# Optimization experiments

Hardware: AMD Instinct MI355X
Metric: run time of the kernel (lower is better)

## Reference

```python
import jax, jax.numpy as jnp
import numpy as np

B, S, H = 128, 512, 256
STEP = 1


def setup_inputs() -> dict:
    key = jax.random.key(0)
    ks = jax.random.split(key, 16)
    stdv = 1.0 / np.sqrt(H)
    u = lambda k, shape: jax.random.uniform(k, shape, jnp.float32, -stdv, stdv)
    return {
        "A": jax.random.uniform(ks[0], (B, S, 2 * S), jnp.float32),
        "hidden": jax.random.normal(ks[1], (B, S, H), jnp.float32),
        "mask": jnp.ones((B, S), jnp.int32),
        # linear_edge_in / linear_edge_out (Linear(H, H, bias=True))
        "W_in": u(ks[2], (H, H)),  "b_in": u(ks[3], (H,)),
        "W_out": u(ks[4], (H, H)), "b_out": u(ks[5], (H,)),
        # adjacency biases
        "b_iah": u(ks[6], (H,)), "b_oah": u(ks[7], (H,)),
        # GRU-style gate weights: w_ih [3H, 2H], w_hh [3H, H]
        "w_ih": u(ks[8], (3 * H, 2 * H)), "b_ih": u(ks[9], (3 * H,)),
        "w_hh": u(ks[10], (3 * H, H)),    "b_hh": u(ks[11], (3 * H,)),
    }


def _gnn_cell(A, hidden, W_in, b_in, W_out, b_out, b_iah, b_oah,
              w_ih, b_ih, w_hh, b_hh):
    s = hidden.shape[1]
    # edge-transformed features (torch F.linear: x @ W.T + b)
    h_in = jnp.einsum('bsh,gh->bsg', hidden, W_in) + b_in
    h_out = jnp.einsum('bsh,gh->bsg', hidden, W_out) + b_out
    # adjacency message passing: [B,S,S] @ [B,S,H]
    input_in = jnp.einsum('bij,bjh->bih', A[:, :, :s], h_in) + b_iah
    input_out = jnp.einsum('bij,bjh->bih', A[:, :, s:2 * s], h_out) + b_oah
    inputs = jnp.concatenate([input_in, input_out], axis=2)  # [B,S,2H]
    gi = jnp.einsum('bsi,gi->bsg', inputs, w_ih) + b_ih      # [B,S,3H]
    gh = jnp.einsum('bsh,gh->bsg', hidden, w_hh) + b_hh      # [B,S,3H]
    i_r, i_i, i_n = jnp.split(gi, 3, axis=2)
    h_r, h_i, h_n = jnp.split(gh, 3, axis=2)
    resetgate = jax.nn.sigmoid(i_r + h_r)
    inputgate = jax.nn.sigmoid(i_i + h_i)
    newgate = jnp.tanh(i_n + resetgate * h_n)
    return hidden + inputgate * (newgate - hidden)


def reference(A, hidden, mask, W_in, b_in, W_out, b_out, b_iah, b_oah,
              w_ih, b_ih, w_hh, b_hh):
    # GNN.forward with issrgnn=True: run GNNCell `step` times (mask unused)
    for _ in range(STEP):
        hidden = _gnn_cell(A, hidden, W_in, b_in, W_out, b_out,
                           b_iah, b_oah, w_ih, b_ih, w_hh, b_hh)
    return hidden
```

## Files before the change

kernel.cpp:

```cpp
#include <hip/hip_runtime.h>

#define B_ 128
#define S_ 512
#define H_ 256
#define M_ (B_*S_)

typedef __attribute__((ext_vector_type(4))) float f32x4;
typedef __attribute__((ext_vector_type(8))) short s16x8;
typedef __attribute__((ext_vector_type(4))) unsigned short u16x4;
typedef unsigned short ushort_t;

typedef __attribute__((address_space(1))) void as1_void;
typedef __attribute__((address_space(3))) void as3_void;

__device__ __forceinline__ unsigned short f2h(float f) {
  _Float16 h = (_Float16)f;
  return __builtin_bit_cast(unsigned short, h);
}

__device__ __forceinline__ f32x4 mfma16(s16x8 a, s16x8 b, f32x4 c) {
  asm("v_mfma_f32_16x16x32_f16 %0, %1, %2, %0" : "+v"(c) : "v"(a), "v"(b));
  return c;
}

__device__ __forceinline__ void cp16(const void* g, void* l) {
  __builtin_amdgcn_global_load_lds((as1_void*)g, (as3_void*)l, 16, 0, 0);
}

__device__ __forceinline__ void waitvm(int n) {
  switch (n) {
    case 0:  asm volatile("s_waitcnt vmcnt(0)"  ::: "memory"); break;
    case 4:  asm volatile("s_waitcnt vmcnt(4)"  ::: "memory"); break;
    case 5:  asm volatile("s_waitcnt vmcnt(5)"  ::: "memory"); break;
    case 6:  asm volatile("s_waitcnt vmcnt(6)"  ::: "memory"); break;
    case 8:  asm volatile("s_waitcnt vmcnt(8)"  ::: "memory"); break;
    case 12: asm volatile("s_waitcnt vmcnt(12)" ::: "memory"); break;
  }
}

__device__ __forceinline__ int stage_kc(int lane) {
  return (lane & 3) ^ ((lane >> 3) & 3);
}
__device__ __forceinline__ int frag_off(int s, int lane) {
  int ln = lane & 15, kg = lane >> 4;
  return s * 512 + (ln * 4 + (kg ^ ((ln >> 1) & 3))) * 8;
}

__global__ void k_cvt_f16(const float* __restrict__ in, ushort_t* __restrict__ out, int n8) {
  int i = blockIdx.x * blockDim.x + threadIdx.x;
  if (i >= n8) return;
  const float* p = in + (size_t)i * 8;
  f32x4 a = *(const f32x4*)p;
  f32x4 b = *(const f32x4*)(p + 4);
  s16x8 o;
  o[0]=(short)f2h(a[0]); o[1]=(short)f2h(a[1]); o[2]=(short)f2h(a[2]); o[3]=(short)f2h(a[3]);
  o[4]=(short)f2h(b[0]); o[5]=(short)f2h(b[1]); o[6]=(short)f2h(b[2]); o[7]=(short)f2h(b[3]);
  *(s16x8*)(out + (size_t)i * 8) = o;
}

__global__ __launch_bounds__(256, 2)
void k_gemm1(const ushort_t* __restrict__ hid, const ushort_t* __restrict__ wcat,
             const float* __restrict__ b_in, const float* __restrict__ b_out,
             ushort_t* __restrict__ hcatT) {
  __shared__ __attribute__((aligned(16))) ushort_t lA[3][8*512];
  __shared__ __attribute__((aligned(16))) ushort_t lB[3][16*512];
  const int flat = blockIdx.y * 8 + blockIdx.x;
  const int orig = (flat & 7) * 128 + (flat >> 3);
  const int bx = orig & 7, bb = orig >> 3;
  const int j0 = (bx >> 1) * 128;
  const int n0 = (bx & 1) * 256;
  const int tid = threadIdx.x;
  const int w = tid >> 6, lane = tid & 63;
  const int ln = lane & 15, kg = lane >> 4;
  const int wm = w >> 1, wn = w & 1;
  const int srow = lane >> 2, skc = stage_kc(lane);

  f32x4 acc[4][8];
  #pragma unroll
  for (int i = 0; i < 4; ++i)
    #pragma unroll
    for (int j = 0; j < 8; ++j) acc[i][j] = (f32x4){0.f,0.f,0.f,0.f};

  const size_t arow0 = (size_t)bb * 512 + j0;

  auto stage = [&](int t, int bsel) {
    int k0 = t * 32;
    #pragma unroll
    for (int it = 0; it < 2; ++it) {
      int s = it*4 + w;
      cp16(hid + (arow0 + s*16 + srow)*256 + k0 + skc*8, &lA[bsel][s*512]);
    }
    #pragma unroll
    for (int it = 0; it < 4; ++it) {
      int s = it*4 + w;
      cp16(wcat + (size_t)(n0 + s*16 + srow)*256 + k0 + skc*8, &lB[bsel][s*512]);
    }
  };
  auto compute = [&](int cur) {
    s16x8 af[4];
    #pragma unroll
    for (int mf = 0; mf < 4; ++mf)
      af[mf] = *(const s16x8*)&lA[cur][frag_off(wm*4 + mf, lane)];
    __builtin_amdgcn_s_setprio(1);
    #pragma unroll
    for (int nf = 0; nf < 8; ++nf) {
      s16x8 bf = *(const s16x8*)&lB[cur][frag_off(wn*8 + nf, lane)];
      #pragma unroll
      for (int mf = 0; mf < 4; ++mf) acc[mf][nf] = mfma16(af[mf], bf, acc[mf][nf]);
    }
    __builtin_amdgcn_s_setprio(0);
  };

  stage(0, 0); stage(1, 1);
  for (int t = 0; t < 6; ++t) {
    waitvm(6);
    __builtin_amdgcn_s_barrier();
    stage(t + 2, (t + 2) % 3);
    compute(t % 3);
  }
  waitvm(6); __builtin_amdgcn_s_barrier(); compute(6 % 3);
  waitvm(0); __builtin_amdgcn_s_barrier(); compute(7 % 3);

  #pragma unroll
  for (int nf = 0; nf < 8; ++nf) {
    int gn = n0 + wn*128 + nf*16 + ln;
    float bias = (gn < 256) ? b_in[gn] : b_out[gn - 256];
    #pragma unroll
    for (int mf = 0; mf < 4; ++mf) {
      int j = j0 + wm*64 + mf*16 + kg*4;
      u16x4 v;
      #pragma unroll
      for (int r = 0; r < 4; ++r) v[r] = f2h(acc[mf][nf][r] + bias);
      *(u16x4*)&hcatT[((size_t)(bb*512 + gn))*512 + j] = v;
    }
  }
}

__global__ __launch_bounds__(256, 2)
void k_gemm2(const float* __restrict__ A, const ushort_t* __restrict__ hcatT,
             const float* __restrict__ b_iah, const float* __restrict__ b_oah,
             ushort_t* __restrict__ inp) {
  __shared__ __attribute__((aligned(16))) ushort_t lA[2][8*512];
  __shared__ __attribute__((aligned(16))) ushort_t lB[3][16*512];
  const int flat = blockIdx.y * 8 + blockIdx.x;
  const int orig = (flat & 7) * 128 + (flat >> 3);
  const int bx = orig & 7, bb = orig >> 3;
  const int i0 = (bx >> 1) * 128;
  const int half = bx & 1;
  const int n0 = half * 256;
  const int tid = threadIdx.x;
  const int w = tid >> 6, lane = tid & 63;
  const int ln = lane & 15, kg = lane >> 4;
  const int wm = w >> 1, wn = w & 1;
  const int srow = lane >> 2, skc = stage_kc(lane);

  f32x4 acc[4][8];
  #pragma unroll
  for (int i = 0; i < 4; ++i)
    #pragma unroll
    for (int j = 0; j < 8; ++j) acc[i][j] = (f32x4){0.f,0.f,0.f,0.f};

  const float* Abase = A + ((size_t)bb*512 + i0)*1024 + half*512;
  f32x4 ra[2][4];

  auto loadA = [&](int t, f32x4 (&r)[4]) {
    int k0 = t * 32;
    #pragma unroll
    for (int it = 0; it < 2; ++it) {
      int s = it*4 + w;
      const float* p = Abase + (size_t)(s*16 + srow)*1024 + k0 + skc*8;
      r[it*2]   = *(const f32x4*)p;
      r[it*2+1] = *(const f32x4*)(p + 4);
    }
  };
  auto stageB = [&](int t, int bsel) {
    int k0 = t * 32;
    #pragma unroll
    for (int it = 0; it < 4; ++it) {
      int s = it*4 + w;
      cp16(hcatT + ((size_t)(bb*512 + n0 + s*16 + srow))*512 + k0 + skc*8, &lB[bsel][s*512]);
    }
  };
  auto writeA = [&](const f32x4 (&r)[4], int bsel) {
    #pragma unroll
    for (int it = 0; it < 2; ++it) {
      int s = it*4 + w;
      s16x8 o;
      o[0]=(short)f2h(r[it*2][0]); o[1]=(short)f2h(r[it*2][1]);
      o[2]=(short)f2h(r[it*2][2]); o[3]=(short)f2h(r[it*2][3]);
      o[4]=(short)f2h(r[it*2+1][0]); o[5]=(short)f2h(r[it*2+1][1]);
      o[6]=(short)f2h(r[it*2+1][2]); o[7]=(short)f2h(r[it*2+1][3]);
      *(s16x8*)&lA[bsel][s*512 + lane*8] = o;
    }
  };
  auto compute = [&](int acur, int bcur) {
    s16x8 af[4];
    #pragma unroll
    for (int mf = 0; mf < 4; ++mf)
      af[mf] = *(const s16x8*)&lA[acur][frag_off(wm*4 + mf, lane)];
    __builtin_amdgcn_s_setprio(1);
    #pragma unroll
    for (int nf = 0; nf < 8; ++nf) {
      s16x8 bf = *(const s16x8*)&lB[bcur][frag_off(wn*8 + nf, lane)];
      #pragma unroll
      for (int mf = 0; mf < 4; ++mf) acc[mf][nf] = mfma16(af[mf], bf, acc[mf][nf]);
    }
    __builtin_amdgcn_s_setprio(0);
  };

  loadA(0, ra[0]); stageB(0, 0);
  loadA(1, ra[1]); stageB(1, 1);
  waitvm(12);
  writeA(ra[0], 0);
  asm volatile("s_waitcnt lgkmcnt(0)" ::: "memory");

  #pragma unroll
  for (int t = 0; t < 16; ++t) {
    waitvm(t < 15 ? 8 : 0);
    __builtin_amdgcn_s_barrier();
    if (t + 2 < 16) { loadA(t + 2, ra[t & 1]); stageB(t + 2, (t + 2) % 3); }
    compute(t & 1, t % 3);
    if (t + 1 < 16) {
      waitvm(t + 2 < 16 ? 12 : 4);
      writeA(ra[(t + 1) & 1], (t + 1) & 1);
      asm volatile("s_waitcnt lgkmcnt(0)" ::: "memory");
    }
  }

  #pragma unroll
  for (int nf = 0; nf < 8; ++nf) {
    int gn = n0 + wn*128 + nf*16 + ln;
    float bias = half ? b_oah[gn - 256] : b_iah[gn];
    #pragma unroll
    for (int mf = 0; mf < 4; ++mf) {
      #pragma unroll
      for (int r = 0; r < 4; ++r) {
        int i = i0 + wm*64 + mf*16 + kg*4 + r;
        inp[((size_t)(bb*512 + i))*512 + gn] = f2h(acc[mf][nf][r] + bias);
      }
    }
  }
}

__global__ __launch_bounds__(256, 2)
void k_gemm3(const ushort_t* __restrict__ inp, const ushort_t* __restrict__ hidh,
             const ushort_t* __restrict__ wih, const ushort_t* __restrict__ whh,
             const float* __restrict__ b_ih, const float* __restrict__ b_hh,
             const float* __restrict__ hidden, float* __restrict__ out) {
  __shared__ __attribute__((aligned(16))) ushort_t lIn[3][8*512];
  __shared__ __attribute__((aligned(16))) ushort_t lW[3][12*512];
  const int flat = blockIdx.y * 4 + blockIdx.x;
  const int orig = (flat & 7) * 256 + (flat >> 3);
  const int h0 = (orig & 3) * 64;
  const int m0 = (orig >> 2) * 128;
  const int tid = threadIdx.x;
  const int w = tid >> 6, lane = tid & 63;
  const int ln = lane & 15, kg = lane >> 4;
  const int wm2 = w >> 1, wh = w & 1;
  const int srow = lane >> 2, skc = stage_kc(lane);

  f32x4 aR[4][2], aI[4][2], aIN[4][2], aHN[4][2];
  #pragma unroll
  for (int m = 0; m < 4; ++m)
    #pragma unroll
    for (int n = 0; n < 2; ++n) {
      aR[m][n] = (f32x4){0.f,0.f,0.f,0.f}; aI[m][n] = (f32x4){0.f,0.f,0.f,0.f};
      aIN[m][n] = (f32x4){0.f,0.f,0.f,0.f}; aHN[m][n] = (f32x4){0.f,0.f,0.f,0.f};
    }

  auto stage = [&](int gs, int bsel) {
    if (gs < 16) {
      int k0 = gs * 32;
      #pragma unroll
      for (int it = 0; it < 2; ++it) {
        int s = it*4 + w;
        cp16(inp + (size_t)(m0 + s*16 + srow)*512 + k0 + skc*8, &lIn[bsel][s*512]);
      }
      #pragma unroll
      for (int it = 0; it < 3; ++it) {
        int s = it*4 + w;
        int row = s*16 + srow, g = row >> 6, r = row & 63;
        cp16(wih + (size_t)(g*256 + h0 + r)*512 + k0 + skc*8, &lW[bsel][s*512]);
      }
    } else {
      int k0 = (gs - 16) * 32;
      #pragma unroll
      for (int it = 0; it < 2; ++it) {
        int s = it*4 + w;
        cp16(hidh + (size_t)(m0 + s*16 + srow)*256 + k0 + skc*8, &lIn[bsel][s*512]);
      }
      #pragma unroll
      for (int it = 0; it < 3; ++it) {
        int s = it*4 + w;
        int row = s*16 + srow, g = row >> 6, r = row & 63;
        cp16(whh + (size_t)(g*256 + h0 + r)*256 + k0 + skc*8, &lW[bsel][s*512]);
      }
    }
  };

  auto compute = [&](int cur, f32x4 (&aN)[4][2]) {
    s16x8 af[4];
    #pragma unroll
    for (int mf = 0; mf < 4; ++mf)
      af[mf] = *(const s16x8*)&lIn[cur][frag_off(wm2*4 + mf, lane)];
    __builtin_amdgcn_s_setprio(1);
    #pragma unroll
    for (int g = 0; g < 3; ++g) {
      #pragma unroll
      for (int nf = 0; nf < 2; ++nf) {
        s16x8 bf = *(const s16x8*)&lW[cur][frag_off(g*4 + wh*2 + nf, lane)];
        #pragma unroll
        for (int mf = 0; mf < 4; ++mf) {
          f32x4& a = (g == 0 ? aR[mf][nf] : g == 1 ? aI[mf][nf] : aN[mf][nf]);
          a = mfma16(af[mf], bf, a);
        }
      }
    }
    __builtin_amdgcn_s_setprio(0);
  };

  stage(0, 0);
  stage(1, 1);
  for (int t = 0; t < 16; ++t) {
    waitvm(5);
    __builtin_amdgcn_s_barrier();
    stage(t + 2, (t + 2) % 3);
    compute(t % 3, aIN);
  }
  for (int t = 16; t < 22; ++t) {
    waitvm(5);
    __builtin_amdgcn_s_barrier();
    stage(t + 2, (t + 2) % 3);
    compute(t % 3, aHN);
  }
  waitvm(5); __builtin_amdgcn_s_barrier(); compute(22 % 3, aHN);
  waitvm(0); __builtin_amdgcn_s_barrier(); compute(23 % 3, aHN);

  #pragma unroll
  for (int nf = 0; nf < 2; ++nf) {
    int h = h0 + wh*32 + nf*16 + ln;
    float br  = b_ih[h]       + b_hh[h];
    float bi  = b_ih[256 + h] + b_hh[256 + h];
    float bni = b_ih[512 + h];
    float bnh = b_hh[512 + h];
    #pragma unroll
    for (int mf = 0; mf < 4; ++mf) {
      #pragma unroll
      for (int r = 0; r < 4; ++r) {
        int m = m0 + wm2*64 + mf*16 + kg*4 + r;
        float rg = 1.0f / (1.0f + __expf(-(aR[mf][nf][r] + br)));
        float ig = 1.0f / (1.0f + __expf(-(aI[mf][nf][r] + bi)));
        float narg = aIN[mf][nf][r] + bni + rg * (aHN[mf][nf][r] + bnh);
        float e2 = __expf(2.0f * narg);
        float ng = 1.0f - 2.0f / (e2 + 1.0f);
        float hv = hidden[(size_t)m*256 + h];
        out[(size_t)m*256 + h] = hv + ig * (ng - hv);
      }
    }
  }
}

extern "C" void kernel_launch(void* const* d_in, const int* in_sizes, int n_in,
                              void* d_out, int out_size, void* d_ws, size_t ws_size,
                              hipStream_t stream) {
  const float* A      = (const float*)d_in[0];
  const float* hidden = (const float*)d_in[1];
  const float* W_in   = (const float*)d_in[3];
  const float* b_in   = (const float*)d_in[4];
  const float* W_out  = (const float*)d_in[5];
  const float* b_out  = (const float*)d_in[6];
  const float* b_iah  = (const float*)d_in[7];
  const float* b_oah  = (const float*)d_in[8];
  const float* w_ih   = (const float*)d_in[9];
  const float* b_ih   = (const float*)d_in[10];
  const float* w_hh   = (const float*)d_in[11];
  const float* b_hh   = (const float*)d_in[12];
  float* out = (float*)d_out;

  char* ws = (char*)d_ws;
  ushort_t* hidh  = (ushort_t*)(ws);
  ushort_t* wcat  = (ushort_t*)(ws + 33554432);
  ushort_t* wihh  = (ushort_t*)(ws + 33816576);
  ushort_t* whhh  = (ushort_t*)(ws + 34603008);
  ushort_t* hcatT = (ushort_t*)(ws + 34996224);
  ushort_t* inp   = (ushort_t*)(ws + 102105088);

  k_cvt_f16<<<8192, 256, 0, stream>>>(hidden, hidh, M_*H_/8);
  k_cvt_f16<<<32,   256, 0, stream>>>(W_in,  wcat,           H_*H_/8);
  k_cvt_f16<<<32,   256, 0, stream>>>(W_out, wcat + H_*H_,   H_*H_/8);
  k_cvt_f16<<<192,  256, 0, stream>>>(w_ih,  wihh, 768*512/8);
  k_cvt_f16<<<96,   256, 0, stream>>>(w_hh,  whhh, 768*256/8);

  k_gemm1<<<dim3(8, 128), 256, 0, stream>>>(hidh, wcat, b_in, b_out, hcatT);
  k_gemm2<<<dim3(8, 128), 256, 0, stream>>>(A, hcatT, b_iah, b_oah, inp);
  k_gemm3<<<dim3(4, 512), 256, 0, stream>>>(inp, hidh, wihh, whhh, b_ih, b_hh, hidden, out);
}
```

Before: 283.4 us.

## Halve gemm3 N-tile to 32 hidden columns and merge conversion kernels into one launch

Measured after the change: 286.5 us. About the same (+1.1%).

```diff
diff --git a/kernel.cpp b/kernel.cpp
--- a/kernel.cpp
+++ b/kernel.cpp
@@ -30,6 +30,7 @@
 __device__ __forceinline__ void waitvm(int n) {
   switch (n) {
     case 0:  asm volatile("s_waitcnt vmcnt(0)"  ::: "memory"); break;
+    case 3:  asm volatile("s_waitcnt vmcnt(3)"  ::: "memory"); break;
     case 4:  asm volatile("s_waitcnt vmcnt(4)"  ::: "memory"); break;
     case 5:  asm volatile("s_waitcnt vmcnt(5)"  ::: "memory"); break;
     case 6:  asm volatile("s_waitcnt vmcnt(6)"  ::: "memory"); break;
@@ -46,16 +47,26 @@
   return s * 512 + (ln * 4 + (kg ^ ((ln >> 1) & 3))) * 8;
 }
 
-__global__ void k_cvt_f16(const float* __restrict__ in, ushort_t* __restrict__ out, int n8) {
-  int i = blockIdx.x * blockDim.x + threadIdx.x;
-  if (i >= n8) return;
-  const float* p = in + (size_t)i * 8;
+__global__ void k_cvt_all(const float* __restrict__ hidden, ushort_t* __restrict__ hidh,
+                          const float* __restrict__ W_in,  const float* __restrict__ W_out,
+                          ushort_t* __restrict__ wcat,
+                          const float* __restrict__ w_ih, ushort_t* __restrict__ wihh,
+                          const float* __restrict__ w_hh, ushort_t* __restrict__ whhh) {
+  int blk = blockIdx.x;
+  const float* src; ushort_t* dst; int base;
+  if (blk < 8192)      { src = hidden; dst = hidh;           base = blk; }
+  else if (blk < 8224) { src = W_in;   dst = wcat;           base = blk - 8192; }
+  else if (blk < 8256) { src = W_out;  dst = wcat + 65536;   base = blk - 8224; }
+  else if (blk < 8448) { src = w_ih;   dst = wihh;           base = blk - 8256; }
+  else                 { src = w_hh;   dst = whhh;           base = blk - 8448; }
+  int i = base * 256 + threadIdx.x;
+  const float* p = src + (size_t)i * 8;
   f32x4 a = *(const f32x4*)p;
   f32x4 b = *(const f32x4*)(p + 4);
   s16x8 o;
   o[0]=(short)f2h(a[0]); o[1]=(short)f2h(a[1]); o[2]=(short)f2h(a[2]); o[3]=(short)f2h(a[3]);
   o[4]=(short)f2h(b[0]); o[5]=(short)f2h(b[1]); o[6]=(short)f2h(b[2]); o[7]=(short)f2h(b[3]);
-  *(s16x8*)(out + (size_t)i * 8) = o;
+  *(s16x8*)(dst + (size_t)i * 8) = o;
 }
 
 __global__ __launch_bounds__(256, 2)
@@ -242,31 +253,29 @@
   }
 }
 
-__global__ __launch_bounds__(256, 2)
+__global__ __launch_bounds__(256, 3)
 void k_gemm3(const ushort_t* __restrict__ inp, const ushort_t* __restrict__ hidh,
              const ushort_t* __restrict__ wih, const ushort_t* __restrict__ whh,
              const float* __restrict__ b_ih, const float* __restrict__ b_hh,
              const float* __restrict__ hidden, float* __restrict__ out) {
   __shared__ __attribute__((aligned(16))) ushort_t lIn[3][8*512];
-  __shared__ __attribute__((aligned(16))) ushort_t lW[3][12*512];
-  const int flat = blockIdx.y * 4 + blockIdx.x;
-  const int orig = (flat & 7) * 256 + (flat >> 3);
-  const int h0 = (orig & 3) * 64;
-  const int m0 = (orig >> 2) * 128;
+  __shared__ __attribute__((aligned(16))) ushort_t lW[3][6*512];
+  const int flat = blockIdx.y * 8 + blockIdx.x;
+  const int orig = (flat & 7) * 512 + (flat >> 3);
+  const int h0 = (orig & 7) * 32;
+  const int m0 = (orig >> 3) * 128;
   const int tid = threadIdx.x;
   const int w = tid >> 6, lane = tid & 63;
   const int ln = lane & 15, kg = lane >> 4;
   const int wm2 = w >> 1, wh = w & 1;
   const int srow = lane >> 2, skc = stage_kc(lane);
 
-  f32x4 aR[4][2], aI[4][2], aIN[4][2], aHN[4][2];
-  #pragma unroll
-  for (int m = 0; m < 4; ++m)
-    #pragma unroll
-    for (int n = 0; n < 2; ++n) {
-      aR[m][n] = (f32x4){0.f,0.f,0.f,0.f}; aI[m][n] = (f32x4){0.f,0.f,0.f,0.f};
-      aIN[m][n] = (f32x4){0.f,0.f,0.f,0.f}; aHN[m][n] = (f32x4){0.f,0.f,0.f,0.f};
-    }
+  f32x4 aR[4], aI[4], aIN[4], aHN[4];
+  #pragma unroll
+  for (int m = 0; m < 4; ++m) {
+    aR[m] = (f32x4){0.f,0.f,0.f,0.f}; aI[m] = (f32x4){0.f,0.f,0.f,0.f};
+    aIN[m] = (f32x4){0.f,0.f,0.f,0.f}; aHN[m] = (f32x4){0.f,0.f,0.f,0.f};
+  }
 
   auto stage = [&](int gs, int bsel) {
     if (gs < 16) {
@@ -277,10 +286,12 @@
         cp16(inp + (size_t)(m0 + s*16 + srow)*512 + k0 + skc*8, &lIn[bsel][s*512]);
       }
       #pragma unroll
-      for (int it = 0; it < 3; ++it) {
+      for (int it = 0; it < 2; ++it) {
         int s = it*4 + w;
-        int row = s*16 + srow, g = row >> 6, r = row & 63;
-        cp16(wih + (size_t)(g*256 + h0 + r)*512 + k0 + skc*8, &lW[bsel][s*512]);
+        if (s < 6) {
+          int g = s >> 1, hh = (s & 1)*16 + srow;
+          cp16(wih + (size_t)(g*256 + h0 + hh)*512 + k0 + skc*8, &lW[bsel][s*512]);
+        }
       }
     } else {
       int k0 = (gs - 16) * 32;
@@ -290,15 +301,17 @@
         cp16(hidh + (size_t)(m0 + s*16 + srow)*256 + k0 + skc*8, &lIn[bsel][s*512]);
       }
       #pragma unroll
-      for (int it = 0; it < 3; ++it) {
+      for (int it = 0; it < 2; ++it) {
         int s = it*4 + w;
-        int row = s*16 + srow, g = row >> 6, r = row & 63;
-        cp16(whh + (size_t)(g*256 + h0 + r)*256 + k0 + skc*8, &lW[bsel][s*512]);
-      }
-    }
-  };
-
-  auto compute = [&](int cur, f32x4 (&aN)[4][2]) {
+        if (s < 6) {
+          int g = s >> 1, hh = (s & 1)*16 + srow;
+          cp16(whh + (size_t)(g*256 + h0 + hh)*256 + k0 + skc*8, &lW[bsel][s*512]);
+        }
+      }
+    }
+  };
+
+  auto compute = [&](int cur, f32x4 (&aN)[4]) {
     s16x8 af[4];
     #pragma unroll
     for (int mf = 0; mf < 4; ++mf)
@@ -306,14 +319,11 @@
     __builtin_amdgcn_s_setprio(1);
     #pragma unroll
     for (int g = 0; g < 3; ++g) {
-      #pragma unroll
-      for (int nf = 0; nf < 2; ++nf) {
-        s16x8 bf = *(const s16x8*)&lW[cur][frag_off(g*4 + wh*2 + nf, lane)];
-        #pragma unroll
-        for (int mf = 0; mf < 4; ++mf) {
-          f32x4& a = (g == 0 ? aR[mf][nf] : g == 1 ? aI[mf][nf] : aN[mf][nf]);
-          a = mfma16(af[mf], bf, a);
-        }
+      s16x8 bf = *(const s16x8*)&lW[cur][frag_off(g*2 + wh, lane)];
+      #pragma unroll
+      for (int mf = 0; mf < 4; ++mf) {
+        f32x4& a = (g == 0 ? aR[mf] : g == 1 ? aI[mf] : aN[mf]);
+        a = mfma16(af[mf], bf, a);
       }
     }
     __builtin_amdgcn_s_setprio(0);
@@ -322,23 +332,21 @@
   stage(0, 0);
   stage(1, 1);
   for (int t = 0; t < 16; ++t) {
-    waitvm(5);
+    if (w < 2) waitvm(5); else waitvm(4);
     __builtin_amdgcn_s_barrier();
     stage(t + 2, (t + 2) % 3);
     compute(t % 3, aIN);
   }
-  for (int t = 16; t < 22; ++t) {
-    waitvm(5);
+  for (int t = 16; t < 23; ++t) {
+    if (w < 2) waitvm(5); else waitvm(4);
     __builtin_amdgcn_s_barrier();
-    stage(t + 2, (t + 2) % 3);
+    if (t + 2 < 24) stage(t + 2, (t + 2) % 3);
     compute(t % 3, aHN);
   }
-  waitvm(5); __builtin_amdgcn_s_barrier(); compute(22 % 3, aHN);
   waitvm(0); __builtin_amdgcn_s_barrier(); compute(23 % 3, aHN);
 
-  #pragma unroll
-  for (int nf = 0; nf < 2; ++nf) {
-    int h = h0 + wh*32 + nf*16 + ln;
+  {
+    int h = h0 + wh*16 + ln;
     float br  = b_ih[h]       + b_hh[h];
     float bi  = b_ih[256 + h] + b_hh[256 + h];
     float bni = b_ih[512 + h];
@@ -348,9 +356,9 @@
       #pragma unroll
       for (int r = 0; r < 4; ++r) {
         int m = m0 + wm2*64 + mf*16 + kg*4 + r;
-        float rg = 1.0f / (1.0f + __expf(-(aR[mf][nf][r] + br)));
-        float ig = 1.0f / (1.0f + __expf(-(aI[mf][nf][r] + bi)));
-        float narg = aIN[mf][nf][r] + bni + rg * (aHN[mf][nf][r] + bnh);
+        float rg = 1.0f / (1.0f + __expf(-(aR[mf][r] + br)));
+        float ig = 1.0f / (1.0f + __expf(-(aI[mf][r] + bi)));
+        float narg = aIN[mf][r] + bni + rg * (aHN[mf][r] + bnh);
         float e2 = __expf(2.0f * narg);
         float ng = 1.0f - 2.0f / (e2 + 1.0f);
         float hv = hidden[(size_t)m*256 + h];
@@ -385,13 +393,10 @@
   ushort_t* hcatT = (ushort_t*)(ws + 34996224);
   ushort_t* inp   = (ushort_t*)(ws + 102105088);
 
-  k_cvt_f16<<<8192, 256, 0, stream>>>(hidden, hidh, M_*H_/8);
-  k_cvt_f16<<<32,   256, 0, stream>>>(W_in,  wcat,           H_*H_/8);
-  k_cvt_f16<<<32,   256, 0, stream>>>(W_out, wcat + H_*H_,   H_*H_/8);
-  k_cvt_f16<<<192,  256, 0, stream>>>(w_ih,  wihh, 768*512/8);
-  k_cvt_f16<<<96,   256, 0, stream>>>(w_hh,  whhh, 768*256/8);
+  k_cvt_all<<<8544, 256, 0, stream>>>(hidden, hidh, W_in, W_out, wcat,
+                                      w_ih, wihh, w_hh, whhh);
 
   k_gemm1<<<dim3(8, 128), 256, 0, stream>>>(hidh, wcat, b_in, b_out, hcatT);
   k_gemm2<<<dim3(8, 128), 256, 0, stream>>>(A, hcatT, b_iah, b_oah, inp);
-  k_gemm3<<<dim3(4, 512), 256, 0, stream>>>(inp, hidh, wihh, whhh, b_ih, b_hh, hidden, out);
-}
+  k_gemm3<<<dim3(8, 512), 256, 0, stream>>>(inp, hidh, wihh, whhh, b_ih, b_hh, hidden, out);
+}
```
